# Kernel tuning notes

Measured on AMD Instinct MI355X. Metric: run time of the kernel, lower is better.

## Reference

```python
import jax, jax.numpy as jnp
import numpy as np

ALPHA = 0.2   # LeakyReLU negative slope
NEG = -1e9    # mask value for non-edges


def setup_inputs() -> dict:
    key = jax.random.key(0)
    ks = jax.random.split(key, 8)
    N, Din, F, H, Dout = 4096, 512, 64, 8, 16
    adj = (jax.random.uniform(ks[0], (N, N)) < 0.01).astype(jnp.float32)
    adjacency = jnp.maximum(adj, jnp.eye(N, dtype=jnp.float32))
    X = jax.random.normal(ks[1], (N, Din), jnp.float32)
    s = lambda k, shape, fan: jax.random.normal(k, shape, jnp.float32) / np.float32(np.sqrt(fan))
    W = s(ks[2], (H, Din, F), Din)        # per-head projection, stacked
    a1 = s(ks[3], (H, F), F)              # attention vector, source half
    a2 = s(ks[4], (H, F), F)              # attention vector, target half
    Wo = s(ks[5], (H * F, Dout), H * F)   # output-layer projection
    ao1 = s(ks[6], (Dout,), Dout)
    ao2 = s(ks[7], (Dout,), Dout)
    return dict(adjacency=adjacency, X=X, W=W, a1=a1, a2=a2, Wo=Wo, ao1=ao1, ao2=ao2)


def reference(adjacency, X, W, a1, a2, Wo, ao1, ao2):
    # dropout is identity (eval mode / p=0)
    mask = adjacency > 0
    N = X.shape[0]
    # --- multi-head attention layers (concat=True -> ELU) ---
    Wh = jnp.einsum('nd,hdf->hnf', X, W)                      # [H, N, F]
    f1 = jnp.einsum('hnf,hf->hn', Wh, a1)                     # [H, N]
    f2 = jnp.einsum('hnf,hf->hn', Wh, a2)                     # [H, N]
    e = jax.nn.leaky_relu(f1[:, :, None] + f2[:, None, :], ALPHA)  # [H, N, N]
    att = jax.nn.softmax(jnp.where(mask[None], e, NEG), axis=-1)
    heads = jax.nn.elu(jnp.einsum('hnm,hmf->hnf', att, Wh))   # [H, N, F]
    cat = jnp.transpose(heads, (1, 0, 2)).reshape(N, -1)      # [N, H*F]
    # --- output attention layer (concat=False -> no ELU) ---
    Who = cat @ Wo                                            # [N, Dout]
    eo = jax.nn.leaky_relu((Who @ ao1)[:, None] + (Who @ ao2)[None, :], ALPHA)
    atto = jax.nn.softmax(jnp.where(mask, eo, NEG), axis=-1)  # [N, N]
    return atto @ Who                                         # [N, Dout]
```

## Files before the change

### kernel.cpp

```cpp
#include <hip/hip_runtime.h>
#include <hip/hip_bf16.h>

#define N_NODES 4096
#define DIN     512
#define FDIM    64
#define NHEADS  8
#define DOUT    16
#define MAXN    512

typedef __attribute__((ext_vector_type(8))) short bf16x8;
typedef __attribute__((ext_vector_type(4))) float f32x4;

static __device__ __forceinline__ float us2f(unsigned short u) {
    union { unsigned int i; float f; } cv; cv.i = ((unsigned int)u) << 16; return cv.f;
}
static __device__ __forceinline__ unsigned short f2us(float v) {
    __hip_bfloat16 b = __float2bfloat16(v);
    return *(const unsigned short*)&b;
}
static __device__ __forceinline__ int is_f32(const void* adj) {
    return (((const unsigned short*)adj)[0] == 0) ? 1 : 0;
}

__global__ __launch_bounds__(256) void prep_kernel(
    const void* __restrict__ adj, const void* __restrict__ X, const void* __restrict__ W,
    const void* __restrict__ a1, const void* __restrict__ a2, const void* __restrict__ Wo,
    const void* __restrict__ ao1, const void* __restrict__ ao2,
    unsigned short* __restrict__ Xhi, unsigned short* __restrict__ Xlo,
    unsigned short* __restrict__ Wt,
    unsigned short* __restrict__ WtH, unsigned short* __restrict__ WtL,
    float* __restrict__ a1c, float* __restrict__ a2c,
    float* __restrict__ ao1c, float* __restrict__ ao2c)
{
    const int f32 = is_f32(adj);
    const int i0 = blockIdx.x * 256 + threadIdx.x;
    const int T = gridDim.x * 256;
    for (int i = i0; i < N_NODES * DIN; i += T) {
        float v = f32 ? ((const float*)X)[i] : us2f(((const unsigned short*)X)[i]);
        unsigned short hi = f2us(v);
        Xhi[i] = hi;
        Xlo[i] = f2us(v - us2f(hi));
    }
    for (int i = i0; i < NHEADS * DIN * FDIM; i += T) {
        int hh = i >> 15, rem = i & 32767, d = rem >> 6, f = rem & 63;
        float v = f32 ? ((const float*)W)[i] : us2f(((const unsigned short*)W)[i]);
        Wt[((size_t)(hh * FDIM + f)) * DIN + d] = f2us(v);
    }
    for (int i = i0; i < DIN * DOUT; i += T) {
        int d = i >> 4, j = i & 15;
        float v = f32 ? ((const float*)Wo)[i] : us2f(((const unsigned short*)Wo)[i]);
        unsigned short hi = f2us(v);
        WtH[j * DIN + d] = hi;
        WtL[j * DIN + d] = f2us(v - us2f(hi));
    }
    if (i0 < 512) {
        a1c[i0] = f32 ? ((const float*)a1)[i0] : us2f(((const unsigned short*)a1)[i0]);
        a2c[i0] = f32 ? ((const float*)a2)[i0] : us2f(((const unsigned short*)a2)[i0]);
    }
    if (i0 < 16) {
        ao1c[i0] = f32 ? ((const float*)ao1)[i0] : us2f(((const unsigned short*)ao1)[i0]);
        ao2c[i0] = f32 ? ((const float*)ao2)[i0] : us2f(((const unsigned short*)ao2)[i0]);
    }
}

__global__ __launch_bounds__(256) void build_nbr_kernel(
    const void* __restrict__ adj, int* __restrict__ cnt, int* __restrict__ nbr)
{
    const int n = blockIdx.x;
    const int f32 = is_f32(adj);
    __shared__ int c;
    if (threadIdx.x == 0) c = 0;
    __syncthreads();
    if (f32) {
        const uint4* row = (const uint4*)((const unsigned int*)adj + (size_t)n * N_NODES);
        for (int q = threadIdx.x; q < N_NODES / 4; q += 256) {
            uint4 v = row[q];
            int base = q * 4;
            if (v.x) { int p = atomicAdd(&c, 1); if (p < MAXN) nbr[(size_t)n * MAXN + p] = base + 0; }
            if (v.y) { int p = atomicAdd(&c, 1); if (p < MAXN) nbr[(size_t)n * MAXN + p] = base + 1; }
            if (v.z) { int p = atomicAdd(&c, 1); if (p < MAXN) nbr[(size_t)n * MAXN + p] = base + 2; }
            if (v.w) { int p = atomicAdd(&c, 1); if (p < MAXN) nbr[(size_t)n * MAXN + p] = base + 3; }
        }
    } else {
        const ushort4* row = (const ushort4*)((const unsigned short*)adj + (size_t)n * N_NODES);
        for (int q = threadIdx.x; q < N_NODES / 4; q += 256) {
            ushort4 v = row[q];
            int base = q * 4;
            if (v.x) { int p = atomicAdd(&c, 1); if (p < MAXN) nbr[(size_t)n * MAXN + p] = base + 0; }
            if (v.y) { int p = atomicAdd(&c, 1); if (p < MAXN) nbr[(size_t)n * MAXN + p] = base + 1; }
            if (v.z) { int p = atomicAdd(&c, 1); if (p < MAXN) nbr[(size_t)n * MAXN + p] = base + 2; }
            if (v.w) { int p = atomicAdd(&c, 1); if (p < MAXN) nbr[(size_t)n * MAXN + p] = base + 3; }
        }
    }
    __syncthreads();
    if (threadIdx.x == 0) cnt[n] = (c < MAXN) ? c : MAXN;
}

__global__ __launch_bounds__(256) void wh_mfma_kernel(
    const unsigned short* __restrict__ Xhi, const unsigned short* __restrict__ Xlo,
    const unsigned short* __restrict__ Wt, unsigned short* __restrict__ Whb)
{
    const int h  = blockIdx.x;
    const int bm = blockIdx.y;
    const int w    = threadIdx.x >> 6;
    const int lane = threadIdx.x & 63;
    const int quad = lane >> 4;
    const int l16  = lane & 15;
    const int rowA = bm * 64 + w * 16 + l16;

    f32x4 acc[4];
#pragma unroll
    for (int j = 0; j < 4; ++j) acc[j] = (f32x4){0.f, 0.f, 0.f, 0.f};

    const unsigned short* xh = Xhi + (size_t)rowA * DIN + quad * 8;
    const unsigned short* xl = Xlo + (size_t)rowA * DIN + quad * 8;
    const unsigned short* wb = Wt + (size_t)h * FDIM * DIN + quad * 8;
#pragma unroll 2
    for (int k0 = 0; k0 < DIN; k0 += 32) {
        bf16x8 ah = *(const bf16x8*)(xh + k0);
        bf16x8 al = *(const bf16x8*)(xl + k0);
#pragma unroll
        for (int j = 0; j < 4; ++j) {
            bf16x8 b = *(const bf16x8*)(wb + (size_t)(j * 16 + l16) * DIN + k0);
            acc[j] = __builtin_amdgcn_mfma_f32_16x16x32_bf16(ah, b, acc[j], 0, 0, 0);
            acc[j] = __builtin_amdgcn_mfma_f32_16x16x32_bf16(al, b, acc[j], 0, 0, 0);
        }
    }
#pragma unroll
    for (int j = 0; j < 4; ++j) {
        int col = j * 16 + l16;
#pragma unroll
        for (int rr = 0; rr < 4; ++rr) {
            int row = bm * 64 + w * 16 + quad * 4 + rr;
            Whb[((size_t)row * NHEADS + h) * FDIM + col] = f2us(acc[j][rr]);
        }
    }
}

__global__ __launch_bounds__(256) void f12_kernel(
    const unsigned short* __restrict__ Whb,
    const float* __restrict__ a1c, const float* __restrict__ a2c,
    float* __restrict__ f1, float* __restrict__ f2)
{
    __shared__ float sA1[512], sA2[512];
    for (int i = threadIdx.x; i < 512; i += 256) {
        int hh = i & 7, ff = i >> 3;
        sA1[i] = a1c[hh * FDIM + ff];
        sA2[i] = a2c[hh * FDIM + ff];
    }
    __syncthreads();
    int idx = blockIdx.x * 256 + threadIdx.x;
    int h = idx & 7, n = idx >> 3;
    const bf16x8* row = (const bf16x8*)(Whb + (size_t)idx * FDIM);
    float s1 = 0.f, s2 = 0.f;
#pragma unroll
    for (int q = 0; q < 8; ++q) {
        bf16x8 v8 = row[q];
#pragma unroll
        for (int t = 0; t < 8; ++t) {
            float v = us2f((unsigned short)v8[t]);
            int f = q * 8 + t;
            s1 += v * sA1[f * 8 + h];
            s2 += v * sA2[f * 8 + h];
        }
    }
    f1[h * N_NODES + n] = s1;
    f2[h * N_NODES + n] = s2;
}

__global__ __launch_bounds__(256) void attn1_kernel(
    const unsigned short* __restrict__ Whb,
    const float* __restrict__ f1, const float* __restrict__ f2,
    const int* __restrict__ cnt, const int* __restrict__ nbr,
    unsigned short* __restrict__ catb)
{
    const int n = blockIdx.x;
    const int tid = threadIdx.x;
    __shared__ int sh_m[MAXN];
    __shared__ float sh_s[NHEADS][MAXN];
    __shared__ float sh_inv[NHEADS];
    const int c0 = cnt[n];
    const int c = (c0 < MAXN) ? c0 : MAXN;
    for (int k = tid; k < c; k += 256) sh_m[k] = nbr[(size_t)n * MAXN + k];
    __syncthreads();
    const int h = tid >> 5;
    const int l32 = tid & 31;
    const float f1v = f1[h * N_NODES + n];
    float mx = -1e30f;
    for (int k = l32; k < c; k += 32) {
        float s = f1v + f2[h * N_NODES + sh_m[k]];
        s = (s >= 0.f) ? s : 0.2f * s;
        sh_s[h][k] = s;
        mx = fmaxf(mx, s);
    }
#pragma unroll
    for (int off = 16; off; off >>= 1) mx = fmaxf(mx, __shfl_xor(mx, off));
    __syncthreads();
    float sum = 0.f;
    for (int k = l32; k < c; k += 32) {
        float e = __expf(sh_s[h][k] - mx);
        sh_s[h][k] = e;
        sum += e;
    }
#pragma unroll
    for (int off = 16; off; off >>= 1) sum += __shfl_xor(sum, off);
    if (l32 == 0) sh_inv[h] = (sum > 0.f) ? 1.f / sum : 0.f;
    __syncthreads();
    float a0 = 0.f, a1v = 0.f;
    const unsigned int* base = (const unsigned int*)Whb;
#pragma unroll 4
    for (int k = 0; k < c; ++k) {
        unsigned int u = base[(size_t)sh_m[k] * 256 + tid];
        float wgt = sh_s[h][k];
        a0  += wgt * us2f((unsigned short)(u & 0xFFFFu));
        a1v += wgt * us2f((unsigned short)(u >> 16));
    }
    const float inv = sh_inv[h];
    a0 *= inv; a1v *= inv;
    a0  = (a0  > 0.f) ? a0  : expm1f(a0);
    a1v = (a1v > 0.f) ? a1v : expm1f(a1v);
    unsigned int o = (unsigned int)f2us(a0) | ((unsigned int)f2us(a1v) << 16);
    ((unsigned int*)catb)[(size_t)n * 256 + tid] = o;
}

__global__ __launch_bounds__(64) void who_mfma_g_kernel(
    const unsigned short* __restrict__ catb,
    const unsigned short* __restrict__ WtH, const unsigned short* __restrict__ WtL,
    const float* __restrict__ ao1c, const float* __restrict__ ao2c,
    float* __restrict__ Who, float* __restrict__ g1, float* __restrict__ g2)
{
    const int lane = threadIdx.x;
    const int quad = lane >> 4, l16 = lane & 15;
    const int row0 = blockIdx.x * 16;
    f32x4 acc = (f32x4){0.f, 0.f, 0.f, 0.f};
    for (int k0 = 0; k0 < DIN; k0 += 32) {
        bf16x8 a  = *(const bf16x8*)&catb[(size_t)(row0 + l16) * DIN + k0 + quad * 8];
        bf16x8 bh = *(const bf16x8*)&WtH[l16 * DIN + k0 + quad * 8];
        bf16x8 bl = *(const bf16x8*)&WtL[l16 * DIN + k0 + quad * 8];
        acc = __builtin_amdgcn_mfma_f32_16x16x32_bf16(a, bh, acc, 0, 0, 0);
        acc = __builtin_amdgcn_mfma_f32_16x16x32_bf16(a, bl, acc, 0, 0, 0);
    }
#pragma unroll
    for (int rr = 0; rr < 4; ++rr) {
        int row = row0 + quad * 4 + rr;
        float v = acc[rr];
        Who[row * DOUT + l16] = v;
        float p1 = v * ao1c[l16];
        float p2 = v * ao2c[l16];
#pragma unroll
        for (int off = 8; off; off >>= 1) {
            p1 += __shfl_xor(p1, off);
            p2 += __shfl_xor(p2, off);
        }
        if (l16 == 0) { g1[row] = p1; g2[row] = p2; }
    }
}

__global__ __launch_bounds__(64) void attn2_kernel(
    const void* __restrict__ adj,
    const float* __restrict__ Who,
    const float* __restrict__ g1, const float* __restrict__ g2,
    const int* __restrict__ cnt, const int* __restrict__ nbr,
    void* __restrict__ out)
{
    const int n = blockIdx.x;
    const int lane = threadIdx.x;
    const int quad = lane >> 4, l16 = lane & 15;
    __shared__ float sh_s[MAXN];
    __shared__ int sh_m[MAXN];
    const int c0 = cnt[n];
    const int c = (c0 < MAXN) ? c0 : MAXN;
    for (int k = lane; k < c; k += 64) sh_m[k] = nbr[(size_t)n * MAXN + k];
    __syncthreads();
    const float gn = g1[n];
    float mx = -1e30f;
    for (int k = lane; k < c; k += 64) {
        float s = gn + g2[sh_m[k]];
        s = (s >= 0.f) ? s : 0.2f * s;
        sh_s[k] = s;
        mx = fmaxf(mx, s);
    }
#pragma unroll
    for (int off = 32; off; off >>= 1) mx = fmaxf(mx, __shfl_xor(mx, off));
    __syncthreads();
    float sum = 0.f;
    for (int k = lane; k < c; k += 64) {
        float e = __expf(sh_s[k] - mx);
        sh_s[k] = e;
        sum += e;
    }
#pragma unroll
    for (int off = 32; off; off >>= 1) sum += __shfl_xor(sum, off);
    __syncthreads();
    const float inv = (sum > 0.f) ? 1.f / sum : 0.f;
    float accv = 0.f;
    for (int k = quad; k < c; k += 4)
        accv += sh_s[k] * Who[sh_m[k] * DOUT + l16];
    accv += __shfl_xor(accv, 16);
    accv += __shfl_xor(accv, 32);
    if (quad == 0) {
        float v = accv * inv;
        if (is_f32(adj)) ((float*)out)[n * DOUT + l16] = v;
        else             ((unsigned short*)out)[n * DOUT + l16] = f2us(v);
    }
}

__global__ void wsfail_kernel(float* __restrict__ out)
{
    if (threadIdx.x == 0) out[0] = 129.f;
}

extern "C" void kernel_launch(void* const* d_in, const int* in_sizes, int n_in,
                              void* d_out, int out_size, void* d_ws, size_t ws_size,
                              hipStream_t stream)
{
    const void* adj = d_in[0];
    const void* X   = d_in[1];
    const void* W   = d_in[2];
    const void* a1  = d_in[3];
    const void* a2  = d_in[4];
    const void* Wo  = d_in[5];
    const void* ao1 = d_in[6];
    const void* ao2 = d_in[7];

    const size_t NEEDED = 26400000;
    if (ws_size < NEEDED) { wsfail_kernel<<<1, 64, 0, stream>>>((float*)d_out); return; }

    int*   cnt  = (int*)d_ws;
    int*   nbr  = cnt + 4096;
    float* a1c  = (float*)(nbr + 2097152);
    float* a2c  = a1c + 512;
    float* ao1c = a2c + 512;
    float* ao2c = ao1c + 16;
    float* f1   = ao2c + 16;
    float* f2   = f1 + 32768;
    float* Who  = f2 + 32768;
    float* g1   = Who + 65536;
    float* g2   = g1 + 4096;
    unsigned short* Whb  = (unsigned short*)(g2 + 4096);
    unsigned short* catb = Whb + 2097152;
    unsigned short* Xhi  = catb + 2097152;
    unsigned short* Xlo  = Xhi + 2097152;
    unsigned short* Wt   = Xlo + 2097152;
    unsigned short* WtH  = Wt + 262144;
    unsigned short* WtL  = WtH + 8192;

    prep_kernel<<<1024, 256, 0, stream>>>(adj, X, W, a1, a2, Wo, ao1, ao2,
                                          Xhi, Xlo, Wt, WtH, WtL, a1c, a2c, ao1c, ao2c);
    build_nbr_kernel<<<N_NODES, 256, 0, stream>>>(adj, cnt, nbr);
    wh_mfma_kernel<<<dim3(NHEADS, N_NODES / 64), 256, 0, stream>>>(Xhi, Xlo, Wt, Whb);
    f12_kernel<<<128, 256, 0, stream>>>(Whb, a1c, a2c, f1, f2);
    attn1_kernel<<<N_NODES, 256, 0, stream>>>(Whb, f1, f2, cnt, nbr, catb);
    who_mfma_g_kernel<<<N_NODES / 16, 64, 0, stream>>>(catb, WtH, WtL, ao1c, ao2c, Who, g1, g2);
    attn2_kernel<<<N_NODES, 64, 0, stream>>>(adj, Who, g1, g2, cnt, nbr, d_out);
}
```

Measured before the change: 177.4 us.

## Fuse neighbor build into prep and f1/f2 projection into Wh MFMA kernel

```diff
diff --git a/kernel.cpp b/kernel.cpp
--- a/kernel.cpp
+++ b/kernel.cpp
@@ -22,7 +22,7 @@
     return (((const unsigned short*)adj)[0] == 0) ? 1 : 0;
 }
 
-__global__ __launch_bounds__(256) void prep_kernel(
+__global__ __launch_bounds__(256) void prep_nbr_kernel(
     const void* __restrict__ adj, const void* __restrict__ X, const void* __restrict__ W,
     const void* __restrict__ a1, const void* __restrict__ a2, const void* __restrict__ Wo,
     const void* __restrict__ ao1, const void* __restrict__ ao2,
@@ -30,11 +30,42 @@
     unsigned short* __restrict__ Wt,
     unsigned short* __restrict__ WtH, unsigned short* __restrict__ WtL,
     float* __restrict__ a1c, float* __restrict__ a2c,
-    float* __restrict__ ao1c, float* __restrict__ ao2c)
+    float* __restrict__ ao1c, float* __restrict__ ao2c,
+    int* __restrict__ cnt, int* __restrict__ nbr)
 {
     const int f32 = is_f32(adj);
+    if (blockIdx.x >= 1024) {
+        const int n = blockIdx.x - 1024;
+        __shared__ int c;
+        if (threadIdx.x == 0) c = 0;
+        __syncthreads();
+        if (f32) {
+            const uint4* row = (const uint4*)((const unsigned int*)adj + (size_t)n * N_NODES);
+            for (int q = threadIdx.x; q < N_NODES / 4; q += 256) {
+                uint4 v = row[q];
+                int base = q * 4;
+                if (v.x) { int p = atomicAdd(&c, 1); if (p < MAXN) nbr[(size_t)n * MAXN + p] = base + 0; }
+                if (v.y) { int p = atomicAdd(&c, 1); if (p < MAXN) nbr[(size_t)n * MAXN + p] = base + 1; }
+                if (v.z) { int p = atomicAdd(&c, 1); if (p < MAXN) nbr[(size_t)n * MAXN + p] = base + 2; }
+                if (v.w) { int p = atomicAdd(&c, 1); if (p < MAXN) nbr[(size_t)n * MAXN + p] = base + 3; }
+            }
+        } else {
+            const ushort4* row = (const ushort4*)((const unsigned short*)adj + (size_t)n * N_NODES);
+            for (int q = threadIdx.x; q < N_NODES / 4; q += 256) {
+                ushort4 v = row[q];
+                int base = q * 4;
+                if (v.x) { int p = atomicAdd(&c, 1); if (p < MAXN) nbr[(size_t)n * MAXN + p] = base + 0; }
+                if (v.y) { int p = atomicAdd(&c, 1); if (p < MAXN) nbr[(size_t)n * MAXN + p] = base + 1; }
+                if (v.z) { int p = atomicAdd(&c, 1); if (p < MAXN) nbr[(size_t)n * MAXN + p] = base + 2; }
+                if (v.w) { int p = atomicAdd(&c, 1); if (p < MAXN) nbr[(size_t)n * MAXN + p] = base + 3; }
+            }
+        }
+        __syncthreads();
+        if (threadIdx.x == 0) cnt[n] = (c < MAXN) ? c : MAXN;
+        return;
+    }
     const int i0 = blockIdx.x * 256 + threadIdx.x;
-    const int T = gridDim.x * 256;
+    const int T = 1024 * 256;
     for (int i = i0; i < N_NODES * DIN; i += T) {
         float v = f32 ? ((const float*)X)[i] : us2f(((const unsigned short*)X)[i]);
         unsigned short hi = f2us(v);
@@ -63,42 +94,11 @@
     }
 }
 
-__global__ __launch_bounds__(256) void build_nbr_kernel(
-    const void* __restrict__ adj, int* __restrict__ cnt, int* __restrict__ nbr)
-{
-    const int n = blockIdx.x;
-    const int f32 = is_f32(adj);
-    __shared__ int c;
-    if (threadIdx.x == 0) c = 0;
-    __syncthreads();
-    if (f32) {
-        const uint4* row = (const uint4*)((const unsigned int*)adj + (size_t)n * N_NODES);
-        for (int q = threadIdx.x; q < N_NODES / 4; q += 256) {
-            uint4 v = row[q];
-            int base = q * 4;
-            if (v.x) { int p = atomicAdd(&c, 1); if (p < MAXN) nbr[(size_t)n * MAXN + p] = base + 0; }
-            if (v.y) { int p = atomicAdd(&c, 1); if (p < MAXN) nbr[(size_t)n * MAXN + p] = base + 1; }
-            if (v.z) { int p = atomicAdd(&c, 1); if (p < MAXN) nbr[(size_t)n * MAXN + p] = base + 2; }
-            if (v.w) { int p = atomicAdd(&c, 1); if (p < MAXN) nbr[(size_t)n * MAXN + p] = base + 3; }
-        }
-    } else {
-        const ushort4* row = (const ushort4*)((const unsigned short*)adj + (size_t)n * N_NODES);
-        for (int q = threadIdx.x; q < N_NODES / 4; q += 256) {
-            ushort4 v = row[q];
-            int base = q * 4;
-            if (v.x) { int p = atomicAdd(&c, 1); if (p < MAXN) nbr[(size_t)n * MAXN + p] = base + 0; }
-            if (v.y) { int p = atomicAdd(&c, 1); if (p < MAXN) nbr[(size_t)n * MAXN + p] = base + 1; }
-            if (v.z) { int p = atomicAdd(&c, 1); if (p < MAXN) nbr[(size_t)n * MAXN + p] = base + 2; }
-            if (v.w) { int p = atomicAdd(&c, 1); if (p < MAXN) nbr[(size_t)n * MAXN + p] = base + 3; }
-        }
-    }
-    __syncthreads();
-    if (threadIdx.x == 0) cnt[n] = (c < MAXN) ? c : MAXN;
-}
-
-__global__ __launch_bounds__(256) void wh_mfma_kernel(
+__global__ __launch_bounds__(256) void wh_f12_kernel(
     const unsigned short* __restrict__ Xhi, const unsigned short* __restrict__ Xlo,
-    const unsigned short* __restrict__ Wt, unsigned short* __restrict__ Whb)
+    const unsigned short* __restrict__ Wt,
+    const float* __restrict__ a1c, const float* __restrict__ a2c,
+    unsigned short* __restrict__ Whb, float* __restrict__ f1, float* __restrict__ f2)
 {
     const int h  = blockIdx.x;
     const int bm = blockIdx.y;
@@ -126,46 +126,33 @@
             acc[j] = __builtin_amdgcn_mfma_f32_16x16x32_bf16(al, b, acc[j], 0, 0, 0);
         }
     }
+    float av1[4], av2[4];
 #pragma unroll
     for (int j = 0; j < 4; ++j) {
         int col = j * 16 + l16;
+        av1[j] = a1c[h * FDIM + col];
+        av2[j] = a2c[h * FDIM + col];
 #pragma unroll
         for (int rr = 0; rr < 4; ++rr) {
             int row = bm * 64 + w * 16 + quad * 4 + rr;
             Whb[((size_t)row * NHEADS + h) * FDIM + col] = f2us(acc[j][rr]);
         }
     }
-}
-
-__global__ __launch_bounds__(256) void f12_kernel(
-    const unsigned short* __restrict__ Whb,
-    const float* __restrict__ a1c, const float* __restrict__ a2c,
-    float* __restrict__ f1, float* __restrict__ f2)
-{
-    __shared__ float sA1[512], sA2[512];
-    for (int i = threadIdx.x; i < 512; i += 256) {
-        int hh = i & 7, ff = i >> 3;
-        sA1[i] = a1c[hh * FDIM + ff];
-        sA2[i] = a2c[hh * FDIM + ff];
-    }
-    __syncthreads();
-    int idx = blockIdx.x * 256 + threadIdx.x;
-    int h = idx & 7, n = idx >> 3;
-    const bf16x8* row = (const bf16x8*)(Whb + (size_t)idx * FDIM);
-    float s1 = 0.f, s2 = 0.f;
-#pragma unroll
-    for (int q = 0; q < 8; ++q) {
-        bf16x8 v8 = row[q];
-#pragma unroll
-        for (int t = 0; t < 8; ++t) {
-            float v = us2f((unsigned short)v8[t]);
-            int f = q * 8 + t;
-            s1 += v * sA1[f * 8 + h];
-            s2 += v * sA2[f * 8 + h];
-        }
-    }
-    f1[h * N_NODES + n] = s1;
-    f2[h * N_NODES + n] = s2;
+#pragma unroll
+    for (int rr = 0; rr < 4; ++rr) {
+        float p1 = acc[0][rr] * av1[0] + acc[1][rr] * av1[1] + acc[2][rr] * av1[2] + acc[3][rr] * av1[3];
+        float p2 = acc[0][rr] * av2[0] + acc[1][rr] * av2[1] + acc[2][rr] * av2[2] + acc[3][rr] * av2[3];
+#pragma unroll
+        for (int off = 8; off; off >>= 1) {
+            p1 += __shfl_xor(p1, off);
+            p2 += __shfl_xor(p2, off);
+        }
+        if (l16 == 0) {
+            int row = bm * 64 + w * 16 + quad * 4 + rr;
+            f1[h * N_NODES + row] = p1;
+            f2[h * N_NODES + row] = p2;
+        }
+    }
 }
 
 __global__ __launch_bounds__(256) void attn1_kernel(
@@ -177,7 +164,7 @@
     const int n = blockIdx.x;
     const int tid = threadIdx.x;
     __shared__ int sh_m[MAXN];
-    __shared__ float sh_s[NHEADS][MAXN];
+    __shared__ float sh_s[NHEADS][516];
     __shared__ float sh_inv[NHEADS];
     const int c0 = cnt[n];
     const int c = (c0 < MAXN) ? c0 : MAXN;
@@ -208,7 +195,7 @@
     __syncthreads();
     float a0 = 0.f, a1v = 0.f;
     const unsigned int* base = (const unsigned int*)Whb;
-#pragma unroll 4
+#pragma unroll 8
     for (int k = 0; k < c; ++k) {
         unsigned int u = base[(size_t)sh_m[k] * 256 + tid];
         float wgt = sh_s[h][k];
@@ -294,6 +281,7 @@
     __syncthreads();
     const float inv = (sum > 0.f) ? 1.f / sum : 0.f;
     float accv = 0.f;
+#pragma unroll 4
     for (int k = quad; k < c; k += 4)
         accv += sh_s[k] * Who[sh_m[k] * DOUT + l16];
     accv += __shfl_xor(accv, 16);
@@ -345,11 +333,11 @@
     unsigned short* WtH  = Wt + 262144;
     unsigned short* WtL  = WtH + 8192;
 
-    prep_kernel<<<1024, 256, 0, stream>>>(adj, X, W, a1, a2, Wo, ao1, ao2,
-                                          Xhi, Xlo, Wt, WtH, WtL, a1c, a2c, ao1c, ao2c);
-    build_nbr_kernel<<<N_NODES, 256, 0, stream>>>(adj, cnt, nbr);
-    wh_mfma_kernel<<<dim3(NHEADS, N_NODES / 64), 256, 0, stream>>>(Xhi, Xlo, Wt, Whb);
-    f12_kernel<<<128, 256, 0, stream>>>(Whb, a1c, a2c, f1, f2);
+    prep_nbr_kernel<<<1024 + N_NODES, 256, 0, stream>>>(
+        adj, X, W, a1, a2, Wo, ao1, ao2,
+        Xhi, Xlo, Wt, WtH, WtL, a1c, a2c, ao1c, ao2c, cnt, nbr);
+    wh_f12_kernel<<<dim3(NHEADS, N_NODES / 64), 256, 0, stream>>>(
+        Xhi, Xlo, Wt, a1c, a2c, Whb, f1, f2);
     attn1_kernel<<<N_NODES, 256, 0, stream>>>(Whb, f1, f2, cnt, nbr, catb);
     who_mfma_g_kernel<<<N_NODES / 16, 64, 0, stream>>>(catb, WtH, WtL, ao1c, ao2c, Who, g1, g2);
     attn2_kernel<<<N_NODES, 64, 0, stream>>>(adj, Who, g1, g2, cnt, nbr, d_out);
```

Result: faster. 165.4 us (-6.8%).
